# Kernel tuning notes

Hardware: AMD Instinct MI355X
Metric: run time of the kernel (lower is better)

The kernel has to match this reference:

```python
import jax, jax.numpy as jnp
import numpy as np

B = 2
T = 1024
D_MODEL = 1024
EXPAND = 2
D_INNER = D_MODEL * EXPAND  # 2048
D_STATE = 16
D_CONV = 4
DT_RANK = 64  # ceil(1024/16)


def setup_inputs() -> dict:
    key = jax.random.key(0)
    ks = jax.random.split(key, 9)
    s = 0.02
    x = jax.random.normal(ks[0], (B, T, D_MODEL), jnp.float32)
    in_proj_w = jax.random.normal(ks[1], (2 * D_INNER, D_MODEL), jnp.float32) * s
    conv_w = jax.random.normal(ks[2], (D_INNER, 1, D_CONV), jnp.float32) * 0.1
    conv_b = jax.random.normal(ks[3], (D_INNER,), jnp.float32) * 0.01
    x_proj_w = jax.random.normal(ks[4], (DT_RANK + 2 * D_STATE, D_INNER), jnp.float32) * s
    dt_proj_w = jax.random.normal(ks[5], (D_INNER, DT_RANK), jnp.float32) * s
    dt_proj_b = jax.random.uniform(ks[6], (D_INNER,), jnp.float32, -4.0, -2.0)
    A_log = jnp.log(jnp.tile(jnp.arange(1, D_STATE + 1, dtype=jnp.float32), (D_INNER, 1)))
    D_param = jnp.ones((D_INNER,), jnp.float32)
    out_proj_w = jax.random.normal(ks[7], (D_MODEL, D_INNER), jnp.float32) * s
    return {"x": x, "in_proj_w": in_proj_w, "conv_w": conv_w, "conv_b": conv_b,
            "x_proj_w": x_proj_w, "dt_proj_w": dt_proj_w, "dt_proj_b": dt_proj_b,
            "A_log": A_log, "D_param": D_param, "out_proj_w": out_proj_w}


def reference(x, in_proj_w, conv_w, conv_b, x_proj_w, dt_proj_w, dt_proj_b,
              A_log, D_param, out_proj_w):
    Bsz, Tlen, _ = x.shape
    # input projection -> (B,T,2*d_inner); split into x-branch and gate z
    xz = jnp.einsum('btd,ed->bte', x, in_proj_w)
    xs, z = jnp.split(xz, 2, axis=-1)
    # causal depthwise conv1d: torch pads both sides by d_conv-1 then slices [:T],
    # equivalent to left-pad d_conv-1
    xc = jnp.swapaxes(xs, 1, 2)  # (B, d_inner, T)
    xc = jax.lax.conv_general_dilated(xc, conv_w, window_strides=(1,),
                                      padding=[(D_CONV - 1, 0)],
                                      feature_group_count=D_INNER)
    xc = xc + conv_b[None, :, None]
    xs = jax.nn.silu(jnp.swapaxes(xc, 1, 2))  # (B,T,d_inner)
    A = -jnp.exp(A_log)  # (d_inner, d_state)
    x_dbl = jnp.einsum('bti,ei->bte', xs, x_proj_w)
    dt, Bv, Cv = jnp.split(x_dbl, [DT_RANK, DT_RANK + D_STATE], axis=-1)
    dt = jax.nn.softplus(jnp.einsum('btr,ir->bti', dt, dt_proj_w) + dt_proj_b)
    # selective scan: h_t = exp(dt_t*A)*h_{t-1} + (dt_t*x_t)*B_t ; y_t = <h_t, C_t>
    def step(h, inp):
        dt_t, B_t, C_t, x_t = inp  # (B,Di),(B,Ds),(B,Ds),(B,Di)
        dA = jnp.exp(dt_t[:, :, None] * A[None])        # (B,Di,Ds)
        h = dA * h + (dt_t * x_t)[:, :, None] * B_t[:, None, :]
        y_t = jnp.einsum('bds,bs->bd', h, C_t)
        return h, y_t
    tm = lambda a: jnp.swapaxes(a, 0, 1)  # time-major
    h0 = jnp.zeros((Bsz, D_INNER, D_STATE), x.dtype)
    _, ys = jax.lax.scan(step, h0, (tm(dt), tm(Bv), tm(Cv), tm(xs)))
    y = jnp.swapaxes(ys, 0, 1) + xs * D_param  # (B,T,d_inner)
    y = y * jax.nn.silu(z)
    return jnp.einsum('bti,di->btd', y, out_proj_w)
```

## Files before the change

kernel.cpp:

```cpp
#include <hip/hip_runtime.h>
#include <hip/hip_bf16.h>
#include <math.h>

#define B_SZ 2
#define T_LEN 1024
#define DMODEL 1024
#define DINNER 2048
#define DSTATE 16
#define DCONV 4
#define DTRANK 64
#define MTOK (B_SZ * T_LEN)

#define NC 32
#define CLEN (T_LEN / NC)
#define NCH (B_SZ * DINNER)
#define NSTATES (NCH * DSTATE)

typedef __bf16 bf16x4 __attribute__((ext_vector_type(4)));
typedef __bf16 bf16x8 __attribute__((ext_vector_type(8)));
typedef float  f32x4  __attribute__((ext_vector_type(4)));

__device__ __forceinline__ float sigmoid_f(float v) { return 1.f / (1.f + __expf(-v)); }

__global__ __launch_bounds__(256) void convert3(const float* __restrict__ x,
                                                const float* __restrict__ w_in,
                                                const float* __restrict__ w_out,
                                                __bf16* __restrict__ xb,
                                                __bf16* __restrict__ wb_in,
                                                __bf16* __restrict__ wb_out)
{
    const int gi = blockIdx.x * blockDim.x + threadIdx.x;
    const float* src; __bf16* dst; int o;
    if (gi < 262144)            { src = x;     dst = xb;     o = gi; }
    else if (gi < 786432)       { src = w_in;  dst = wb_in;  o = gi - 262144; }
    else                        { src = w_out; dst = wb_out; o = gi - 786432; }
    float4 a = reinterpret_cast<const float4*>(src)[2 * o];
    float4 b = reinterpret_cast<const float4*>(src)[2 * o + 1];
    bf16x8 v = {(__bf16)a.x, (__bf16)a.y, (__bf16)a.z, (__bf16)a.w,
                (__bf16)b.x, (__bf16)b.y, (__bf16)b.z, (__bf16)b.w};
    reinterpret_cast<bf16x8*>(dst)[o] = v;
}

template<int BN, typename CT>
__global__ __launch_bounds__(256) void mfma_gemm_bf16(const __bf16* __restrict__ A, int lda,
                                                      const __bf16* __restrict__ Bm, int ldb,
                                                      CT* __restrict__ C, int ldc, int K)
{
    constexpr int NF = BN / 32;
    constexpr int BCALLS = BN / 32;
    __shared__ __align__(16) __bf16 As[128 * 64];
    __shared__ __align__(16) __bf16 Bs[BN * 64];
    const int tid  = threadIdx.x;
    const int lane = tid & 63;
    const int w    = tid >> 6;
    const int wr   = w >> 1, wc = w & 1;
    const int m0   = blockIdx.y * 128, n0 = blockIdx.x * BN;

    f32x4 acc[4][NF];
    #pragma unroll
    for (int i = 0; i < 4; ++i)
        #pragma unroll
        for (int j = 0; j < NF; ++j) {
            f32x4 z = {0.f, 0.f, 0.f, 0.f};
            acc[i][j] = z;
        }

    const int fr = lane & 15;
    const int kq = (lane >> 4) * 8;

    for (int k0 = 0; k0 < K; k0 += 64) {
        #pragma unroll
        for (int c = 0; c < 4; ++c) {
            const int idx = c * 256 + tid;
            const int row = idx >> 3;
            const int kc  = (idx & 7) * 8;
            __builtin_amdgcn_global_load_lds(
                (const __attribute__((address_space(1))) unsigned int*)(A + (size_t)(m0 + row) * lda + k0 + kc),
                (__attribute__((address_space(3))) unsigned int*)(As + idx * 8),
                16, 0, 0);
        }
        #pragma unroll
        for (int c = 0; c < BCALLS; ++c) {
            const int idx = c * 256 + tid;
            const int row = idx >> 3;
            const int kc  = (idx & 7) * 8;
            __builtin_amdgcn_global_load_lds(
                (const __attribute__((address_space(1))) unsigned int*)(Bm + (size_t)(n0 + row) * ldb + k0 + kc),
                (__attribute__((address_space(3))) unsigned int*)(Bs + idx * 8),
                16, 0, 0);
        }
        __syncthreads();

        bf16x8 af[4][2], bfr[NF][2];
        #pragma unroll
        for (int i = 0; i < 4; ++i) {
            const __bf16* pa = As + (wr * 64 + i * 16 + fr) * 64 + kq;
            af[i][0] = *reinterpret_cast<const bf16x8*>(pa);
            af[i][1] = *reinterpret_cast<const bf16x8*>(pa + 32);
        }
        #pragma unroll
        for (int j = 0; j < NF; ++j) {
            const __bf16* pb = Bs + (wc * (BN / 2) + j * 16 + fr) * 64 + kq;
            bfr[j][0] = *reinterpret_cast<const bf16x8*>(pb);
            bfr[j][1] = *reinterpret_cast<const bf16x8*>(pb + 32);
        }
        #pragma unroll
        for (int i = 0; i < 4; ++i)
            #pragma unroll
            for (int j = 0; j < NF; ++j) {
                acc[i][j] = __builtin_amdgcn_mfma_f32_16x16x32_bf16(af[i][0], bfr[j][0], acc[i][j], 0, 0, 0);
                acc[i][j] = __builtin_amdgcn_mfma_f32_16x16x32_bf16(af[i][1], bfr[j][1], acc[i][j], 0, 0, 0);
            }
        __syncthreads();
    }

    const int crow = (lane >> 4) * 4;
    const int ccol = lane & 15;
    #pragma unroll
    for (int i = 0; i < 4; ++i)
        #pragma unroll
        for (int j = 0; j < NF; ++j) {
            CT* cp = C + (size_t)(m0 + wr * 64 + i * 16 + crow) * ldc
                       + n0 + wc * (BN / 2) + j * 16 + ccol;
            cp[0 * (size_t)ldc] = (CT)acc[i][j][0];
            cp[1 * (size_t)ldc] = (CT)acc[i][j][1];
            cp[2 * (size_t)ldc] = (CT)acc[i][j][2];
            cp[3 * (size_t)ldc] = (CT)acc[i][j][3];
        }
}

__global__ __launch_bounds__(256) void gemm_dtproj(const float* __restrict__ A,
                                                   const float* __restrict__ Bm,
                                                   __bf16* __restrict__ C,
                                                   const float* __restrict__ bias)
{
    __shared__ float As[16][68];
    __shared__ float Bs[16][68];
    const int tx = threadIdx.x & 15;
    const int ty = threadIdx.x >> 4;
    const int m0 = blockIdx.y * 64;
    const int n0 = blockIdx.x * 64;
    const int lr = threadIdx.x >> 2;
    const int lc = (threadIdx.x & 3) * 4;

    float acc[4][4] = {};

    for (int k0 = 0; k0 < DTRANK; k0 += 16) {
        {
            float4 v = *reinterpret_cast<const float4*>(&A[(size_t)(m0 + lr) * 96 + k0 + lc]);
            As[lc + 0][lr] = v.x; As[lc + 1][lr] = v.y;
            As[lc + 2][lr] = v.z; As[lc + 3][lr] = v.w;
        }
        {
            float4 v = *reinterpret_cast<const float4*>(&Bm[(size_t)(n0 + lr) * DTRANK + k0 + lc]);
            Bs[lc + 0][lr] = v.x; Bs[lc + 1][lr] = v.y;
            Bs[lc + 2][lr] = v.z; Bs[lc + 3][lr] = v.w;
        }
        __syncthreads();
        #pragma unroll
        for (int kk = 0; kk < 16; ++kk) {
            float av[4], bv[4];
            #pragma unroll
            for (int i = 0; i < 4; ++i) av[i] = As[kk][ty + 16 * i];
            #pragma unroll
            for (int j = 0; j < 4; ++j) bv[j] = Bs[kk][tx + 16 * j];
            #pragma unroll
            for (int i = 0; i < 4; ++i)
                #pragma unroll
                for (int j = 0; j < 4; ++j)
                    acc[i][j] = fmaf(av[i], bv[j], acc[i][j]);
        }
        __syncthreads();
    }

    #pragma unroll
    for (int i = 0; i < 4; ++i) {
        int m = m0 + ty + 16 * i;
        #pragma unroll
        for (int j = 0; j < 4; ++j) {
            int n = n0 + tx + 16 * j;
            float v = acc[i][j] + bias[n];
            v = (v > 20.f) ? v : log1pf(__expf(v));
            C[(size_t)m * DINNER + n] = (__bf16)v;
        }
    }
}

#define XP_KS 16
#define XP_KC (DINNER / XP_KS)

__global__ __launch_bounds__(256) void gemm_xproj_splitk(const __bf16* __restrict__ xsb,
                                                         const float* __restrict__ W,
                                                         float* __restrict__ pbuf)
{
    __shared__ float As[16][68];
    __shared__ float Bs[16][68];
    const int tx = threadIdx.x & 15;
    const int ty = threadIdx.x >> 4;
    const int n0 = blockIdx.x * 64;
    const int m0 = blockIdx.y * 64;
    const int kz = blockIdx.z;
    const int lr = threadIdx.x >> 2;
    const int lc = (threadIdx.x & 3) * 4;

    float acc[4][4] = {};

    for (int k0 = kz * XP_KC; k0 < (kz + 1) * XP_KC; k0 += 16) {
        {
            bf16x4 v = *reinterpret_cast<const bf16x4*>(&xsb[(size_t)(m0 + lr) * DINNER + k0 + lc]);
            As[lc + 0][lr] = (float)v[0]; As[lc + 1][lr] = (float)v[1];
            As[lc + 2][lr] = (float)v[2]; As[lc + 3][lr] = (float)v[3];
        }
        {
            int n = n0 + lr;
            float4 v = make_float4(0.f, 0.f, 0.f, 0.f);
            if (n < DTRANK + 2 * DSTATE)
                v = *reinterpret_cast<const float4*>(&W[(size_t)n * DINNER + k0 + lc]);
            Bs[lc + 0][lr] = v.x; Bs[lc + 1][lr] = v.y;
            Bs[lc + 2][lr] = v.z; Bs[lc + 3][lr] = v.w;
        }
        __syncthreads();
        #pragma unroll
        for (int kk = 0; kk < 16; ++kk) {
            float av[4], bv[4];
            #pragma unroll
            for (int i = 0; i < 4; ++i) av[i] = As[kk][ty + 16 * i];
            #pragma unroll
            for (int j = 0; j < 4; ++j) bv[j] = Bs[kk][tx + 16 * j];
            #pragma unroll
            for (int i = 0; i < 4; ++i)
                #pragma unroll
                for (int j = 0; j < 4; ++j)
                    acc[i][j] = fmaf(av[i], bv[j], acc[i][j]);
        }
        __syncthreads();
    }

    float* pc = pbuf + (size_t)kz * MTOK * 96;
    #pragma unroll
    for (int i = 0; i < 4; ++i) {
        int m = m0 + ty + 16 * i;
        #pragma unroll
        for (int j = 0; j < 4; ++j) {
            int n = n0 + tx + 16 * j;
            if (n < 96) pc[(size_t)m * 96 + n] = acc[i][j];
        }
    }
}

__global__ __launch_bounds__(256) void reduce_xproj(const float* __restrict__ pbuf,
                                                    float* __restrict__ xdbl)
{
    const int idx = blockIdx.x * blockDim.x + threadIdx.x;
    const float4* p = reinterpret_cast<const float4*>(pbuf) + idx;
    float4 s = p[0];
    #pragma unroll
    for (int z = 1; z < XP_KS; ++z) {
        float4 v = p[(size_t)z * (MTOK * 96 / 4)];
        s.x += v.x; s.y += v.y; s.z += v.z; s.w += v.w;
    }
    reinterpret_cast<float4*>(xdbl)[idx] = s;
}

__global__ __launch_bounds__(256) void conv_silu_kernel(const __bf16* __restrict__ xzb,
                                                        const float* __restrict__ cw,
                                                        const float* __restrict__ cb,
                                                        __bf16* __restrict__ xsb)
{
    int tid = blockIdx.x * blockDim.x + threadIdx.x;
    int d = tid & (DINNER - 1);
    int t = (tid >> 11) & (T_LEN - 1);
    int b = tid >> 21;
    float acc = cb[d];
    const float4 w = *reinterpret_cast<const float4*>(&cw[d * DCONV]);
    float wv[4] = {w.x, w.y, w.z, w.w};
    #pragma unroll
    for (int j = 0; j < DCONV; ++j) {
        int tt = t - (DCONV - 1) + j;
        if (tt >= 0)
            acc = fmaf((float)xzb[((size_t)(b * T_LEN + tt)) * (2 * DINNER) + d], wv[j], acc);
    }
    xsb[tid] = (__bf16)(acc * sigmoid_f(acc));
}

__global__ __launch_bounds__(256) void scan_pass1(const __bf16* __restrict__ dtb,
                                                  const __bf16* __restrict__ xsb,
                                                  const float* __restrict__ xdbl,
                                                  const float* __restrict__ A_log,
                                                  float* __restrict__ Pb,
                                                  float* __restrict__ Bb)
{
    __shared__ float sB[CLEN][16];
    const int tid = threadIdx.x;
    const int g   = blockIdx.x * 256 + tid;
    const int c   = blockIdx.y;
    const int b   = g >> 11;
    const int d   = g & (DINNER - 1);
    const int m0  = b * T_LEN + c * CLEN;

    if (tid < CLEN * 4) {
        int t = tid >> 2, s4 = (tid & 3) * 4;
        *reinterpret_cast<float4*>(&sB[t][s4]) =
            *reinterpret_cast<const float4*>(&xdbl[(size_t)(m0 + t) * 96 + DTRANK + s4]);
    }
    __syncthreads();

    float a[DSTATE], h[DSTATE];
    #pragma unroll
    for (int s4 = 0; s4 < DSTATE; s4 += 4) {
        float4 v = *reinterpret_cast<const float4*>(&A_log[d * DSTATE + s4]);
        a[s4 + 0] = -__expf(v.x); a[s4 + 1] = -__expf(v.y);
        a[s4 + 2] = -__expf(v.z); a[s4 + 3] = -__expf(v.w);
        h[s4 + 0] = 0.f; h[s4 + 1] = 0.f; h[s4 + 2] = 0.f; h[s4 + 3] = 0.f;
    }

    float sumdt = 0.f;
    float dtc = (float)dtb[(size_t)m0 * DINNER + d];
    float xc  = (float)xsb[(size_t)m0 * DINNER + d];
    for (int t = 0; t < CLEN; ++t) {
        float dtn = 0.f, xn = 0.f;
        if (t + 1 < CLEN) {
            dtn = (float)dtb[(size_t)(m0 + t + 1) * DINNER + d];
            xn  = (float)xsb[(size_t)(m0 + t + 1) * DINNER + d];
        }
        sumdt += dtc;
        const float u = dtc * xc;
        #pragma unroll
        for (int s = 0; s < DSTATE; ++s) {
            const float dA = __expf(dtc * a[s]);
            h[s] = fmaf(dA, h[s], u * sB[t][s]);
        }
        dtc = dtn; xc = xn;
    }

    float* pp = Pb + ((size_t)c * NCH + g) * DSTATE;
    float* bp = Bb + ((size_t)c * NCH + g) * DSTATE;
    #pragma unroll
    for (int s4 = 0; s4 < DSTATE; s4 += 4) {
        float4 pv = {__expf(a[s4] * sumdt), __expf(a[s4 + 1] * sumdt),
                     __expf(a[s4 + 2] * sumdt), __expf(a[s4 + 3] * sumdt)};
        *reinterpret_cast<float4*>(pp + s4) = pv;
        float4 hv = {h[s4], h[s4 + 1], h[s4 + 2], h[s4 + 3]};
        *reinterpret_cast<float4*>(bp + s4) = hv;
    }
}

__global__ __launch_bounds__(256) void scan_pass2(const float* __restrict__ Pb,
                                                  float* __restrict__ Bb)
{
    const int idx = blockIdx.x * blockDim.x + threadIdx.x;
    float h = 0.f;
    #pragma unroll
    for (int c = 0; c < NC; ++c) {
        const size_t o = (size_t)c * NSTATES + idx;
        const float P  = Pb[o];
        const float Bv = Bb[o];
        Bb[o] = h;
        h = fmaf(P, h, Bv);
    }
}

__global__ __launch_bounds__(256) void scan_pass3(const __bf16* __restrict__ dtb,
                                                  const __bf16* __restrict__ xsb,
                                                  const float* __restrict__ xdbl,
                                                  const float* __restrict__ Hs,
                                                  const float* __restrict__ A_log,
                                                  const float* __restrict__ Dp,
                                                  const __bf16* __restrict__ xzb,
                                                  __bf16* __restrict__ yMb)
{
    __shared__ float sBC[CLEN][32];
    const int tid = threadIdx.x;
    const int g   = blockIdx.x * 256 + tid;
    const int c   = blockIdx.y;
    const int b   = g >> 11;
    const int d   = g & (DINNER - 1);
    const int m0  = b * T_LEN + c * CLEN;

    {
        int t = tid >> 3, col = (tid & 7) * 4;
        if (t < CLEN)
            *reinterpret_cast<float4*>(&sBC[t][col]) =
                *reinterpret_cast<const float4*>(&xdbl[(size_t)(m0 + t) * 96 + DTRANK + col]);
    }
    __syncthreads();

    float a[DSTATE], h[DSTATE];
    #pragma unroll
    for (int s4 = 0; s4 < DSTATE; s4 += 4) {
        float4 v = *reinterpret_cast<const float4*>(&A_log[d * DSTATE + s4]);
        a[s4 + 0] = -__expf(v.x); a[s4 + 1] = -__expf(v.y);
        a[s4 + 2] = -__expf(v.z); a[s4 + 3] = -__expf(v.w);
        float4 hv = *reinterpret_cast<const float4*>(
            Hs + ((size_t)c * NCH + g) * DSTATE + s4);
        h[s4 + 0] = hv.x; h[s4 + 1] = hv.y; h[s4 + 2] = hv.z; h[s4 + 3] = hv.w;
    }
    const float Dv = Dp[d];

    float dtc = (float)dtb[(size_t)m0 * DINNER + d];
    float xc  = (float)xsb[(size_t)m0 * DINNER + d];
    float zc  = (float)xzb[(size_t)m0 * (2 * DINNER) + DINNER + d];
    for (int t = 0; t < CLEN; ++t) {
        float dtn = 0.f, xn = 0.f, zn = 0.f;
        if (t + 1 < CLEN) {
            dtn = (float)dtb[(size_t)(m0 + t + 1) * DINNER + d];
            xn  = (float)xsb[(size_t)(m0 + t + 1) * DINNER + d];
            zn  = (float)xzb[(size_t)(m0 + t + 1) * (2 * DINNER) + DINNER + d];
        }
        const float u = dtc * xc;
        float y0 = 0.f, y1 = 0.f, y2 = 0.f, y3 = 0.f;
        #pragma unroll
        for (int s = 0; s < DSTATE; s += 4) {
            float dA0 = __expf(dtc * a[s + 0]);
            float dA1 = __expf(dtc * a[s + 1]);
            float dA2 = __expf(dtc * a[s + 2]);
            float dA3 = __expf(dtc * a[s + 3]);
            h[s + 0] = fmaf(dA0, h[s + 0], u * sBC[t][s + 0]);
            h[s + 1] = fmaf(dA1, h[s + 1], u * sBC[t][s + 1]);
            h[s + 2] = fmaf(dA2, h[s + 2], u * sBC[t][s + 2]);
            h[s + 3] = fmaf(dA3, h[s + 3], u * sBC[t][s + 3]);
            y0 = fmaf(h[s + 0], sBC[t][16 + s + 0], y0);
            y1 = fmaf(h[s + 1], sBC[t][16 + s + 1], y1);
            y2 = fmaf(h[s + 2], sBC[t][16 + s + 2], y2);
            y3 = fmaf(h[s + 3], sBC[t][16 + s + 3], y3);
        }
        float y = (y0 + y1) + (y2 + y3) + xc * Dv;
        const float gate = zc * sigmoid_f(zc);
        yMb[(size_t)(m0 + t) * DINNER + d] = (__bf16)(y * gate);
        dtc = dtn; xc = xn; zc = zn;
    }
}

extern "C" void kernel_launch(void* const* d_in, const int* in_sizes, int n_in,
                              void* d_out, int out_size, void* d_ws, size_t ws_size,
                              hipStream_t stream) {
    const float* x         = (const float*)d_in[0];
    const float* in_proj_w = (const float*)d_in[1];
    const float* conv_w    = (const float*)d_in[2];
    const float* conv_b    = (const float*)d_in[3];
    const float* x_proj_w  = (const float*)d_in[4];
    const float* dt_proj_w = (const float*)d_in[5];
    const float* dt_proj_b = (const float*)d_in[6];
    const float* A_log     = (const float*)d_in[7];
    const float* D_param   = (const float*)d_in[8];
    const float* out_proj_w= (const float*)d_in[9];
    float* out = (float*)d_out;

    float* ws = (float*)d_ws;
    const size_t M1 = (size_t)1024 * 1024;
    __bf16* xzb    = (__bf16*)ws;
    __bf16* xb     = (__bf16*)(ws + 4 * M1);
    __bf16* wb_in  = (__bf16*)(ws + 5 * M1);
    __bf16* wb_out = (__bf16*)(ws + 7 * M1);
    __bf16* xsb    = (__bf16*)(ws + 8 * M1);
    __bf16* dtb    = (__bf16*)(ws + 10 * M1);
    float*  xdbl   = ws + 12 * M1;
    float*  pbuf   = ws + 13 * M1;
    float*  Pb     = ws + 16 * M1;
    float*  Bb     = ws + 18 * M1;
    __bf16* yMb    = (__bf16*)(ws + 20 * M1);

    dim3 blk(256);

    convert3<<<dim3(4096), blk, 0, stream>>>(x, in_proj_w, out_proj_w, xb, wb_in, wb_out);

    mfma_gemm_bf16<128, __bf16><<<dim3((2 * DINNER) / 128, MTOK / 128), blk, 0, stream>>>(
        xb, DMODEL, wb_in, DMODEL, xzb, 2 * DINNER, DMODEL);

    conv_silu_kernel<<<dim3(B_SZ * T_LEN * DINNER / 256), blk, 0, stream>>>(xzb, conv_w, conv_b, xsb);

    gemm_xproj_splitk<<<dim3(2, MTOK / 64, XP_KS), blk, 0, stream>>>(xsb, x_proj_w, pbuf);

    reduce_xproj<<<dim3(MTOK * 96 / 4 / 256), blk, 0, stream>>>(pbuf, xdbl);

    gemm_dtproj<<<dim3(DINNER / 64, MTOK / 64), blk, 0, stream>>>(xdbl, dt_proj_w, dtb, dt_proj_b);

    scan_pass1<<<dim3(NCH / 256, NC), blk, 0, stream>>>(dtb, xsb, xdbl, A_log, Pb, Bb);
    scan_pass2<<<dim3(NSTATES / 256), blk, 0, stream>>>(Pb, Bb);
    scan_pass3<<<dim3(NCH / 256, NC), blk, 0, stream>>>(dtb, xsb, xdbl, Bb, A_log, D_param, xzb, yMb);

    mfma_gemm_bf16<64, float><<<dim3(DMODEL / 64, MTOK / 128), blk, 0, stream>>>(
        yMb, DINNER, wb_out, DINNER, out, DMODEL, DINNER);
}
```

Before: 194.2 us.

## Fuse conv+SiLU into x_proj and scan kernels, replace split-K reduce with atomics

Removes the standalone conv_silu kernel and its xsb buffer. The depthwise causal conv and SiLU are now recomputed on the fly from xzb inside the x_proj GEMM load path and inside both scan passes, using a sliding window of three previous values. The split-K partial buffer and its reduce kernel are replaced by atomic adds into xdbl, which is zeroed by extra blocks of the convert kernel. This saves two launches and a large intermediate write and read, at the cost of redundant conv arithmetic, four-times-wider loads in the GEMM tile fill, and nondeterministic float atomics.

```diff
diff --git a/kernel.cpp b/kernel.cpp
--- a/kernel.cpp
+++ b/kernel.cpp
@@ -27,13 +27,21 @@
                                                 const float* __restrict__ w_out,
                                                 __bf16* __restrict__ xb,
                                                 __bf16* __restrict__ wb_in,
-                                                __bf16* __restrict__ wb_out)
+                                                __bf16* __restrict__ wb_out,
+                                                float* __restrict__ xdbl)
 {
     const int gi = blockIdx.x * blockDim.x + threadIdx.x;
+    if (gi >= 1048576) {
+        const int o = gi - 1048576;
+        float4 z = make_float4(0.f, 0.f, 0.f, 0.f);
+        reinterpret_cast<float4*>(xdbl)[2 * o]     = z;
+        reinterpret_cast<float4*>(xdbl)[2 * o + 1] = z;
+        return;
+    }
     const float* src; __bf16* dst; int o;
-    if (gi < 262144)            { src = x;     dst = xb;     o = gi; }
-    else if (gi < 786432)       { src = w_in;  dst = wb_in;  o = gi - 262144; }
-    else                        { src = w_out; dst = wb_out; o = gi - 786432; }
+    if (gi < 262144)      { src = x;     dst = xb;     o = gi; }
+    else if (gi < 786432) { src = w_in;  dst = wb_in;  o = gi - 262144; }
+    else                  { src = w_out; dst = wb_out; o = gi - 786432; }
     float4 a = reinterpret_cast<const float4*>(src)[2 * o];
     float4 b = reinterpret_cast<const float4*>(src)[2 * o + 1];
     bf16x8 v = {(__bf16)a.x, (__bf16)a.y, (__bf16)a.z, (__bf16)a.w,
@@ -129,69 +137,14 @@
         }
 }
 
-__global__ __launch_bounds__(256) void gemm_dtproj(const float* __restrict__ A,
-                                                   const float* __restrict__ Bm,
-                                                   __bf16* __restrict__ C,
-                                                   const float* __restrict__ bias)
-{
-    __shared__ float As[16][68];
-    __shared__ float Bs[16][68];
-    const int tx = threadIdx.x & 15;
-    const int ty = threadIdx.x >> 4;
-    const int m0 = blockIdx.y * 64;
-    const int n0 = blockIdx.x * 64;
-    const int lr = threadIdx.x >> 2;
-    const int lc = (threadIdx.x & 3) * 4;
-
-    float acc[4][4] = {};
-
-    for (int k0 = 0; k0 < DTRANK; k0 += 16) {
-        {
-            float4 v = *reinterpret_cast<const float4*>(&A[(size_t)(m0 + lr) * 96 + k0 + lc]);
-            As[lc + 0][lr] = v.x; As[lc + 1][lr] = v.y;
-            As[lc + 2][lr] = v.z; As[lc + 3][lr] = v.w;
-        }
-        {
-            float4 v = *reinterpret_cast<const float4*>(&Bm[(size_t)(n0 + lr) * DTRANK + k0 + lc]);
-            Bs[lc + 0][lr] = v.x; Bs[lc + 1][lr] = v.y;
-            Bs[lc + 2][lr] = v.z; Bs[lc + 3][lr] = v.w;
-        }
-        __syncthreads();
-        #pragma unroll
-        for (int kk = 0; kk < 16; ++kk) {
-            float av[4], bv[4];
-            #pragma unroll
-            for (int i = 0; i < 4; ++i) av[i] = As[kk][ty + 16 * i];
-            #pragma unroll
-            for (int j = 0; j < 4; ++j) bv[j] = Bs[kk][tx + 16 * j];
-            #pragma unroll
-            for (int i = 0; i < 4; ++i)
-                #pragma unroll
-                for (int j = 0; j < 4; ++j)
-                    acc[i][j] = fmaf(av[i], bv[j], acc[i][j]);
-        }
-        __syncthreads();
-    }
-
-    #pragma unroll
-    for (int i = 0; i < 4; ++i) {
-        int m = m0 + ty + 16 * i;
-        #pragma unroll
-        for (int j = 0; j < 4; ++j) {
-            int n = n0 + tx + 16 * j;
-            float v = acc[i][j] + bias[n];
-            v = (v > 20.f) ? v : log1pf(__expf(v));
-            C[(size_t)m * DINNER + n] = (__bf16)v;
-        }
-    }
-}
-
 #define XP_KS 16
 #define XP_KC (DINNER / XP_KS)
 
-__global__ __launch_bounds__(256) void gemm_xproj_splitk(const __bf16* __restrict__ xsb,
+__global__ __launch_bounds__(256) void gemm_xproj_splitk(const __bf16* __restrict__ xzb,
+                                                         const float* __restrict__ cw,
+                                                         const float* __restrict__ cb,
                                                          const float* __restrict__ W,
-                                                         float* __restrict__ pbuf)
+                                                         float* __restrict__ xdbl)
 {
     __shared__ float As[16][68];
     __shared__ float Bs[16][68];
@@ -203,13 +156,38 @@
     const int lr = threadIdx.x >> 2;
     const int lc = (threadIdx.x & 3) * 4;
 
+    const int m  = m0 + lr;
+    const int tb = m & (T_LEN - 1);
+
     float acc[4][4] = {};
 
     for (int k0 = kz * XP_KC; k0 < (kz + 1) * XP_KC; k0 += 16) {
         {
-            bf16x4 v = *reinterpret_cast<const bf16x4*>(&xsb[(size_t)(m0 + lr) * DINNER + k0 + lc]);
-            As[lc + 0][lr] = (float)v[0]; As[lc + 1][lr] = (float)v[1];
-            As[lc + 2][lr] = (float)v[2]; As[lc + 3][lr] = (float)v[3];
+            const int ch0 = k0 + lc;
+            float xv[4][4];
+            #pragma unroll
+            for (int j = 0; j < 4; ++j) {
+                if (tb - 3 + j >= 0) {
+                    bf16x4 v = *reinterpret_cast<const bf16x4*>(
+                        &xzb[(size_t)(m - 3 + j) * (2 * DINNER) + ch0]);
+                    xv[j][0] = (float)v[0]; xv[j][1] = (float)v[1];
+                    xv[j][2] = (float)v[2]; xv[j][3] = (float)v[3];
+                } else {
+                    xv[j][0] = xv[j][1] = xv[j][2] = xv[j][3] = 0.f;
+                }
+            }
+            float4 cbv = *reinterpret_cast<const float4*>(&cb[ch0]);
+            float cbw[4] = {cbv.x, cbv.y, cbv.z, cbv.w};
+            #pragma unroll
+            for (int c = 0; c < 4; ++c) {
+                float4 wv = *reinterpret_cast<const float4*>(&cw[(ch0 + c) * DCONV]);
+                float a = cbw[c];
+                a = fmaf(xv[0][c], wv.x, a);
+                a = fmaf(xv[1][c], wv.y, a);
+                a = fmaf(xv[2][c], wv.z, a);
+                a = fmaf(xv[3][c], wv.w, a);
+                As[lc + c][lr] = a * sigmoid_f(a);
+            }
         }
         {
             int n = n0 + lr;
@@ -236,55 +214,78 @@
         __syncthreads();
     }
 
-    float* pc = pbuf + (size_t)kz * MTOK * 96;
+    #pragma unroll
+    for (int i = 0; i < 4; ++i) {
+        int mm = m0 + ty + 16 * i;
+        #pragma unroll
+        for (int j = 0; j < 4; ++j) {
+            int n = n0 + tx + 16 * j;
+            if (n < 96) unsafeAtomicAdd(&xdbl[(size_t)mm * 96 + n], acc[i][j]);
+        }
+    }
+}
+
+__global__ __launch_bounds__(256) void gemm_dtproj(const float* __restrict__ A,
+                                                   const float* __restrict__ Bm,
+                                                   __bf16* __restrict__ C,
+                                                   const float* __restrict__ bias)
+{
+    __shared__ float As[16][68];
+    __shared__ float Bs[16][68];
+    const int tx = threadIdx.x & 15;
+    const int ty = threadIdx.x >> 4;
+    const int m0 = blockIdx.y * 64;
+    const int n0 = blockIdx.x * 64;
+    const int lr = threadIdx.x >> 2;
+    const int lc = (threadIdx.x & 3) * 4;
+
+    float acc[4][4] = {};
+
+    for (int k0 = 0; k0 < DTRANK; k0 += 16) {
+        {
+            float4 v = *reinterpret_cast<const float4*>(&A[(size_t)(m0 + lr) * 96 + k0 + lc]);
+            As[lc + 0][lr] = v.x; As[lc + 1][lr] = v.y;
+            As[lc + 2][lr] = v.z; As[lc + 3][lr] = v.w;
+        }
+        {
+            float4 v = *reinterpret_cast<const float4*>(&Bm[(size_t)(n0 + lr) * DTRANK + k0 + lc]);
+            Bs[lc + 0][lr] = v.x; Bs[lc + 1][lr] = v.y;
+            Bs[lc + 2][lr] = v.z; Bs[lc + 3][lr] = v.w;
+        }
+        __syncthreads();
+        #pragma unroll
+        for (int kk = 0; kk < 16; ++kk) {
+            float av[4], bv[4];
+            #pragma unroll
+            for (int i = 0; i < 4; ++i) av[i] = As[kk][ty + 16 * i];
+            #pragma unroll
+            for (int j = 0; j < 4; ++j) bv[j] = Bs[kk][tx + 16 * j];
+            #pragma unroll
+            for (int i = 0; i < 4; ++i)
+                #pragma unroll
+                for (int j = 0; j < 4; ++j)
+                    acc[i][j] = fmaf(av[i], bv[j], acc[i][j]);
+        }
+        __syncthreads();
+    }
+
     #pragma unroll
     for (int i = 0; i < 4; ++i) {
         int m = m0 + ty + 16 * i;
         #pragma unroll
         for (int j = 0; j < 4; ++j) {
             int n = n0 + tx + 16 * j;
-            if (n < 96) pc[(size_t)m * 96 + n] = acc[i][j];
-        }
-    }
-}
-
-__global__ __launch_bounds__(256) void reduce_xproj(const float* __restrict__ pbuf,
-                                                    float* __restrict__ xdbl)
-{
-    const int idx = blockIdx.x * blockDim.x + threadIdx.x;
-    const float4* p = reinterpret_cast<const float4*>(pbuf) + idx;
-    float4 s = p[0];
-    #pragma unroll
-    for (int z = 1; z < XP_KS; ++z) {
-        float4 v = p[(size_t)z * (MTOK * 96 / 4)];
-        s.x += v.x; s.y += v.y; s.z += v.z; s.w += v.w;
-    }
-    reinterpret_cast<float4*>(xdbl)[idx] = s;
-}
-
-__global__ __launch_bounds__(256) void conv_silu_kernel(const __bf16* __restrict__ xzb,
-                                                        const float* __restrict__ cw,
-                                                        const float* __restrict__ cb,
-                                                        __bf16* __restrict__ xsb)
-{
-    int tid = blockIdx.x * blockDim.x + threadIdx.x;
-    int d = tid & (DINNER - 1);
-    int t = (tid >> 11) & (T_LEN - 1);
-    int b = tid >> 21;
-    float acc = cb[d];
-    const float4 w = *reinterpret_cast<const float4*>(&cw[d * DCONV]);
-    float wv[4] = {w.x, w.y, w.z, w.w};
-    #pragma unroll
-    for (int j = 0; j < DCONV; ++j) {
-        int tt = t - (DCONV - 1) + j;
-        if (tt >= 0)
-            acc = fmaf((float)xzb[((size_t)(b * T_LEN + tt)) * (2 * DINNER) + d], wv[j], acc);
-    }
-    xsb[tid] = (__bf16)(acc * sigmoid_f(acc));
+            float v = acc[i][j] + bias[n];
+            v = (v > 20.f) ? v : log1pf(__expf(v));
+            C[(size_t)m * DINNER + n] = (__bf16)v;
+        }
+    }
 }
 
 __global__ __launch_bounds__(256) void scan_pass1(const __bf16* __restrict__ dtb,
-                                                  const __bf16* __restrict__ xsb,
+                                                  const __bf16* __restrict__ xzb,
+                                                  const float* __restrict__ cw,
+                                                  const float* __restrict__ cb,
                                                   const float* __restrict__ xdbl,
                                                   const float* __restrict__ A_log,
                                                   float* __restrict__ Pb,
@@ -314,15 +315,28 @@
         h[s4 + 0] = 0.f; h[s4 + 1] = 0.f; h[s4 + 2] = 0.f; h[s4 + 3] = 0.f;
     }
 
+    const float4 wv = *reinterpret_cast<const float4*>(&cw[d * DCONV]);
+    const float cbv = cb[d];
+    float xw0, xw1, xw2;
+    if (c > 0) {
+        xw0 = (float)xzb[(size_t)(m0 - 3) * (2 * DINNER) + d];
+        xw1 = (float)xzb[(size_t)(m0 - 2) * (2 * DINNER) + d];
+        xw2 = (float)xzb[(size_t)(m0 - 1) * (2 * DINNER) + d];
+    } else { xw0 = xw1 = xw2 = 0.f; }
+
     float sumdt = 0.f;
     float dtc = (float)dtb[(size_t)m0 * DINNER + d];
-    float xc  = (float)xsb[(size_t)m0 * DINNER + d];
+    float xzc = (float)xzb[(size_t)m0 * (2 * DINNER) + d];
     for (int t = 0; t < CLEN; ++t) {
-        float dtn = 0.f, xn = 0.f;
+        float dtn = 0.f, xzn = 0.f;
         if (t + 1 < CLEN) {
             dtn = (float)dtb[(size_t)(m0 + t + 1) * DINNER + d];
-            xn  = (float)xsb[(size_t)(m0 + t + 1) * DINNER + d];
-        }
+            xzn = (float)xzb[(size_t)(m0 + t + 1) * (2 * DINNER) + d];
+        }
+        float xc = cbv;
+        xc = fmaf(xw0, wv.x, xc); xc = fmaf(xw1, wv.y, xc);
+        xc = fmaf(xw2, wv.z, xc); xc = fmaf(xzc, wv.w, xc);
+        xc = xc * sigmoid_f(xc);
         sumdt += dtc;
         const float u = dtc * xc;
         #pragma unroll
@@ -330,7 +344,8 @@
             const float dA = __expf(dtc * a[s]);
             h[s] = fmaf(dA, h[s], u * sB[t][s]);
         }
-        dtc = dtn; xc = xn;
+        xw0 = xw1; xw1 = xw2; xw2 = xzc;
+        dtc = dtn; xzc = xzn;
     }
 
     float* pp = Pb + ((size_t)c * NCH + g) * DSTATE;
@@ -361,12 +376,13 @@
 }
 
 __global__ __launch_bounds__(256) void scan_pass3(const __bf16* __restrict__ dtb,
-                                                  const __bf16* __restrict__ xsb,
+                                                  const __bf16* __restrict__ xzb,
+                                                  const float* __restrict__ cw,
+                                                  const float* __restrict__ cb,
                                                   const float* __restrict__ xdbl,
                                                   const float* __restrict__ Hs,
                                                   const float* __restrict__ A_log,
                                                   const float* __restrict__ Dp,
-                                                  const __bf16* __restrict__ xzb,
                                                   __bf16* __restrict__ yMb)
 {
     __shared__ float sBC[CLEN][32];
@@ -397,16 +413,29 @@
     }
     const float Dv = Dp[d];
 
+    const float4 wv = *reinterpret_cast<const float4*>(&cw[d * DCONV]);
+    const float cbv = cb[d];
+    float xw0, xw1, xw2;
+    if (c > 0) {
+        xw0 = (float)xzb[(size_t)(m0 - 3) * (2 * DINNER) + d];
+        xw1 = (float)xzb[(size_t)(m0 - 2) * (2 * DINNER) + d];
+        xw2 = (float)xzb[(size_t)(m0 - 1) * (2 * DINNER) + d];
+    } else { xw0 = xw1 = xw2 = 0.f; }
+
     float dtc = (float)dtb[(size_t)m0 * DINNER + d];
-    float xc  = (float)xsb[(size_t)m0 * DINNER + d];
+    float xzc = (float)xzb[(size_t)m0 * (2 * DINNER) + d];
     float zc  = (float)xzb[(size_t)m0 * (2 * DINNER) + DINNER + d];
     for (int t = 0; t < CLEN; ++t) {
-        float dtn = 0.f, xn = 0.f, zn = 0.f;
+        float dtn = 0.f, xzn = 0.f, zn = 0.f;
         if (t + 1 < CLEN) {
             dtn = (float)dtb[(size_t)(m0 + t + 1) * DINNER + d];
-            xn  = (float)xsb[(size_t)(m0 + t + 1) * DINNER + d];
+            xzn = (float)xzb[(size_t)(m0 + t + 1) * (2 * DINNER) + d];
             zn  = (float)xzb[(size_t)(m0 + t + 1) * (2 * DINNER) + DINNER + d];
         }
+        float xc = cbv;
+        xc = fmaf(xw0, wv.x, xc); xc = fmaf(xw1, wv.y, xc);
+        xc = fmaf(xw2, wv.z, xc); xc = fmaf(xzc, wv.w, xc);
+        xc = xc * sigmoid_f(xc);
         const float u = dtc * xc;
         float y0 = 0.f, y1 = 0.f, y2 = 0.f, y3 = 0.f;
         #pragma unroll
@@ -427,7 +456,8 @@
         float y = (y0 + y1) + (y2 + y3) + xc * Dv;
         const float gate = zc * sigmoid_f(zc);
         yMb[(size_t)(m0 + t) * DINNER + d] = (__bf16)(y * gate);
-        dtc = dtn; xc = xn; zc = zn;
+        xw0 = xw1; xw1 = xw2; xw2 = xzc;
+        dtc = dtn; xzc = xzn; zc = zn;
     }
 }
 
@@ -452,32 +482,27 @@
     __bf16* xb     = (__bf16*)(ws + 4 * M1);
     __bf16* wb_in  = (__bf16*)(ws + 5 * M1);
     __bf16* wb_out = (__bf16*)(ws + 7 * M1);
-    __bf16* xsb    = (__bf16*)(ws + 8 * M1);
-    __bf16* dtb    = (__bf16*)(ws + 10 * M1);
-    float*  xdbl   = ws + 12 * M1;
-    float*  pbuf   = ws + 13 * M1;
-    float*  Pb     = ws + 16 * M1;
-    float*  Bb     = ws + 18 * M1;
-    __bf16* yMb    = (__bf16*)(ws + 20 * M1);
+    __bf16* dtb    = (__bf16*)(ws + 8 * M1);
+    float*  xdbl   = ws + 10 * M1;
+    float*  Pb     = ws + 11 * M1;
+    float*  Bb     = ws + 13 * M1;
+    __bf16* yMb    = (__bf16*)(ws + 15 * M1);
 
     dim3 blk(256);
 
-    convert3<<<dim3(4096), blk, 0, stream>>>(x, in_proj_w, out_proj_w, xb, wb_in, wb_out);
+    convert3<<<dim3(4192), blk, 0, stream>>>(x, in_proj_w, out_proj_w, xb, wb_in, wb_out, xdbl);
 
     mfma_gemm_bf16<128, __bf16><<<dim3((2 * DINNER) / 128, MTOK / 128), blk, 0, stream>>>(
         xb, DMODEL, wb_in, DMODEL, xzb, 2 * DINNER, DMODEL);
 
-    conv_silu_kernel<<<dim3(B_SZ * T_LEN * DINNER / 256), blk, 0, stream>>>(xzb, conv_w, conv_b, xsb);
-
-    gemm_xproj_splitk<<<dim3(2, MTOK / 64, XP_KS), blk, 0, stream>>>(xsb, x_proj_w, pbuf);
-
-    reduce_xproj<<<dim3(MTOK * 96 / 4 / 256), blk, 0, stream>>>(pbuf, xdbl);
+    gemm_xproj_splitk<<<dim3(2, MTOK / 64, XP_KS), blk, 0, stream>>>(
+        xzb, conv_w, conv_b, x_proj_w, xdbl);
 
     gemm_dtproj<<<dim3(DINNER / 64, MTOK / 64), blk, 0, stream>>>(xdbl, dt_proj_w, dtb, dt_proj_b);
 
-    scan_pass1<<<dim3(NCH / 256, NC), blk, 0, stream>>>(dtb, xsb, xdbl, A_log, Pb, Bb);
+    scan_pass1<<<dim3(NCH / 256, NC), blk, 0, stream>>>(dtb, xzb, conv_w, conv_b, xdbl, A_log, Pb, Bb);
     scan_pass2<<<dim3(NSTATES / 256), blk, 0, stream>>>(Pb, Bb);
-    scan_pass3<<<dim3(NCH / 256, NC), blk, 0, stream>>>(dtb, xsb, xdbl, Bb, A_log, D_param, xzb, yMb);
+    scan_pass3<<<dim3(NCH / 256, NC), blk, 0, stream>>>(dtb, xzb, conv_w, conv_b, xdbl, Bb, A_log, D_param, yMb);
 
     mfma_gemm_bf16<64, float><<<dim3(DMODEL / 64, MTOK / 128), blk, 0, stream>>>(
         yMb, DINNER, wb_out, DINNER, out, DMODEL, DINNER);
```

Measured after the change: 194.5 us. No clear change (+0.2%).

## Replace FP32 split-K x_proj GEMM and reduction with bf16 MFMA atomic split-K

Applied to the files above, without the earlier changes.

The x_proj projection moves from a scalar FP32 split-K GEMM with a separate reduce kernel to a bf16 MFMA kernel. It loads tiles straight into LDS and accumulates split-K partials into xdbl with float atomics. The x_proj weight conversion to bf16 and the zeroing of xdbl are folded into the existing conversion kernel. This removes one launch and the partial-sum buffer traffic, at the cost of atomic contention, non-deterministic summation order and lower weight precision.

```diff
diff --git a/kernel.cpp b/kernel.cpp
--- a/kernel.cpp
+++ b/kernel.cpp
@@ -16,24 +16,38 @@
 #define NCH (B_SZ * DINNER)
 #define NSTATES (NCH * DSTATE)
 
+#define XPK 8
+#define XPKC (DINNER / XPK)
+
 typedef __bf16 bf16x4 __attribute__((ext_vector_type(4)));
 typedef __bf16 bf16x8 __attribute__((ext_vector_type(8)));
 typedef float  f32x4  __attribute__((ext_vector_type(4)));
 
 __device__ __forceinline__ float sigmoid_f(float v) { return 1.f / (1.f + __expf(-v)); }
 
-__global__ __launch_bounds__(256) void convert3(const float* __restrict__ x,
+__global__ __launch_bounds__(256) void convert4(const float* __restrict__ x,
                                                 const float* __restrict__ w_in,
                                                 const float* __restrict__ w_out,
+                                                const float* __restrict__ w_xp,
                                                 __bf16* __restrict__ xb,
                                                 __bf16* __restrict__ wb_in,
-                                                __bf16* __restrict__ wb_out)
+                                                __bf16* __restrict__ wb_out,
+                                                __bf16* __restrict__ wxp,
+                                                float* __restrict__ xdbl)
 {
     const int gi = blockIdx.x * blockDim.x + threadIdx.x;
+    if (gi >= 1073152) {
+        const int o = gi - 1073152;
+        float4 z = make_float4(0.f, 0.f, 0.f, 0.f);
+        reinterpret_cast<float4*>(xdbl)[2 * o]     = z;
+        reinterpret_cast<float4*>(xdbl)[2 * o + 1] = z;
+        return;
+    }
     const float* src; __bf16* dst; int o;
-    if (gi < 262144)            { src = x;     dst = xb;     o = gi; }
-    else if (gi < 786432)       { src = w_in;  dst = wb_in;  o = gi - 262144; }
-    else                        { src = w_out; dst = wb_out; o = gi - 786432; }
+    if (gi < 262144)       { src = x;     dst = xb;     o = gi; }
+    else if (gi < 786432)  { src = w_in;  dst = wb_in;  o = gi - 262144; }
+    else if (gi < 1048576) { src = w_out; dst = wb_out; o = gi - 786432; }
+    else                   { src = w_xp;  dst = wxp;    o = gi - 1048576; }
     float4 a = reinterpret_cast<const float4*>(src)[2 * o];
     float4 b = reinterpret_cast<const float4*>(src)[2 * o + 1];
     bf16x8 v = {(__bf16)a.x, (__bf16)a.y, (__bf16)a.z, (__bf16)a.w,
@@ -127,6 +141,101 @@
             cp[2 * (size_t)ldc] = (CT)acc[i][j][2];
             cp[3 * (size_t)ldc] = (CT)acc[i][j][3];
         }
+}
+
+__global__ __launch_bounds__(256) void mfma_xproj(const __bf16* __restrict__ A,
+                                                  const __bf16* __restrict__ Bm,
+                                                  float* __restrict__ xdbl)
+{
+    __shared__ __align__(16) __bf16 As[128 * 64];
+    __shared__ __align__(16) __bf16 Bs[32 * 64];
+    const int tid  = threadIdx.x;
+    const int lane = tid & 63;
+    const int w    = tid >> 6;
+    const int wr   = w >> 1, wc = w & 1;
+    const int m0   = blockIdx.y * 128, n0 = blockIdx.x * 32;
+    const int kbeg = blockIdx.z * XPKC;
+
+    f32x4 acc[4];
+    #pragma unroll
+    for (int i = 0; i < 4; ++i) { f32x4 z = {0.f, 0.f, 0.f, 0.f}; acc[i] = z; }
+
+    const int fr = lane & 15;
+    const int kq = (lane >> 4) * 8;
+
+    for (int k0 = kbeg; k0 < kbeg + XPKC; k0 += 64) {
+        #pragma unroll
+        for (int c = 0; c < 4; ++c) {
+            const int idx = c * 256 + tid;
+            const int row = idx >> 3;
+            const int kc  = (idx & 7) * 8;
+            __builtin_amdgcn_global_load_lds(
+                (const __attribute__((address_space(1))) unsigned int*)(A + (size_t)(m0 + row) * DINNER + k0 + kc),
+                (__attribute__((address_space(3))) unsigned int*)(As + idx * 8),
+                16, 0, 0);
+        }
+        {
+            const int row = tid >> 3;
+            const int kc  = (tid & 7) * 8;
+            __builtin_amdgcn_global_load_lds(
+                (const __attribute__((address_space(1))) unsigned int*)(Bm + (size_t)(n0 + row) * DINNER + k0 + kc),
+                (__attribute__((address_space(3))) unsigned int*)(Bs + tid * 8),
+                16, 0, 0);
+        }
+        __syncthreads();
+
+        bf16x8 af[4][2], bfr[2];
+        #pragma unroll
+        for (int i = 0; i < 4; ++i) {
+            const __bf16* pa = As + (wr * 64 + i * 16 + fr) * 64 + kq;
+            af[i][0] = *reinterpret_cast<const bf16x8*>(pa);
+            af[i][1] = *reinterpret_cast<const bf16x8*>(pa + 32);
+        }
+        {
+            const __bf16* pb = Bs + (wc * 16 + fr) * 64 + kq;
+            bfr[0] = *reinterpret_cast<const bf16x8*>(pb);
+            bfr[1] = *reinterpret_cast<const bf16x8*>(pb + 32);
+        }
+        #pragma unroll
+        for (int i = 0; i < 4; ++i) {
+            acc[i] = __builtin_amdgcn_mfma_f32_16x16x32_bf16(af[i][0], bfr[0], acc[i], 0, 0, 0);
+            acc[i] = __builtin_amdgcn_mfma_f32_16x16x32_bf16(af[i][1], bfr[1], acc[i], 0, 0, 0);
+        }
+        __syncthreads();
+    }
+
+    const int crow = (lane >> 4) * 4;
+    const int ccol = lane & 15;
+    const int n = n0 + wc * 16 + ccol;
+    #pragma unroll
+    for (int i = 0; i < 4; ++i) {
+        const int m = m0 + wr * 64 + i * 16 + crow;
+        unsafeAtomicAdd(&xdbl[(size_t)(m + 0) * 96 + n], acc[i][0]);
+        unsafeAtomicAdd(&xdbl[(size_t)(m + 1) * 96 + n], acc[i][1]);
+        unsafeAtomicAdd(&xdbl[(size_t)(m + 2) * 96 + n], acc[i][2]);
+        unsafeAtomicAdd(&xdbl[(size_t)(m + 3) * 96 + n], acc[i][3]);
+    }
+}
+
+__global__ __launch_bounds__(256) void conv_silu_kernel(const __bf16* __restrict__ xzb,
+                                                        const float* __restrict__ cw,
+                                                        const float* __restrict__ cb,
+                                                        __bf16* __restrict__ xsb)
+{
+    int tid = blockIdx.x * blockDim.x + threadIdx.x;
+    int d = tid & (DINNER - 1);
+    int t = (tid >> 11) & (T_LEN - 1);
+    int b = tid >> 21;
+    float acc = cb[d];
+    const float4 w = *reinterpret_cast<const float4*>(&cw[d * DCONV]);
+    float wv[4] = {w.x, w.y, w.z, w.w};
+    #pragma unroll
+    for (int j = 0; j < DCONV; ++j) {
+        int tt = t - (DCONV - 1) + j;
+        if (tt >= 0)
+            acc = fmaf((float)xzb[((size_t)(b * T_LEN + tt)) * (2 * DINNER) + d], wv[j], acc);
+    }
+    xsb[tid] = (__bf16)(acc * sigmoid_f(acc));
 }
 
 __global__ __launch_bounds__(256) void gemm_dtproj(const float* __restrict__ A,
@@ -184,103 +293,6 @@
             C[(size_t)m * DINNER + n] = (__bf16)v;
         }
     }
-}
-
-#define XP_KS 16
-#define XP_KC (DINNER / XP_KS)
-
-__global__ __launch_bounds__(256) void gemm_xproj_splitk(const __bf16* __restrict__ xsb,
-                                                         const float* __restrict__ W,
-                                                         float* __restrict__ pbuf)
-{
-    __shared__ float As[16][68];
-    __shared__ float Bs[16][68];
-    const int tx = threadIdx.x & 15;
-    const int ty = threadIdx.x >> 4;
-    const int n0 = blockIdx.x * 64;
-    const int m0 = blockIdx.y * 64;
-    const int kz = blockIdx.z;
-    const int lr = threadIdx.x >> 2;
-    const int lc = (threadIdx.x & 3) * 4;
-
-    float acc[4][4] = {};
-
-    for (int k0 = kz * XP_KC; k0 < (kz + 1) * XP_KC; k0 += 16) {
-        {
-            bf16x4 v = *reinterpret_cast<const bf16x4*>(&xsb[(size_t)(m0 + lr) * DINNER + k0 + lc]);
-            As[lc + 0][lr] = (float)v[0]; As[lc + 1][lr] = (float)v[1];
-            As[lc + 2][lr] = (float)v[2]; As[lc + 3][lr] = (float)v[3];
-        }
-        {
-            int n = n0 + lr;
-            float4 v = make_float4(0.f, 0.f, 0.f, 0.f);
-            if (n < DTRANK + 2 * DSTATE)
-                v = *reinterpret_cast<const float4*>(&W[(size_t)n * DINNER + k0 + lc]);
-            Bs[lc + 0][lr] = v.x; Bs[lc + 1][lr] = v.y;
-            Bs[lc + 2][lr] = v.z; Bs[lc + 3][lr] = v.w;
-        }
-        __syncthreads();
-        #pragma unroll
-        for (int kk = 0; kk < 16; ++kk) {
-            float av[4], bv[4];
-            #pragma unroll
-            for (int i = 0; i < 4; ++i) av[i] = As[kk][ty + 16 * i];
-            #pragma unroll
-            for (int j = 0; j < 4; ++j) bv[j] = Bs[kk][tx + 16 * j];
-            #pragma unroll
-            for (int i = 0; i < 4; ++i)
-                #pragma unroll
-                for (int j = 0; j < 4; ++j)
-                    acc[i][j] = fmaf(av[i], bv[j], acc[i][j]);
-        }
-        __syncthreads();
-    }
-
-    float* pc = pbuf + (size_t)kz * MTOK * 96;
-    #pragma unroll
-    for (int i = 0; i < 4; ++i) {
-        int m = m0 + ty + 16 * i;
-        #pragma unroll
-        for (int j = 0; j < 4; ++j) {
-            int n = n0 + tx + 16 * j;
-            if (n < 96) pc[(size_t)m * 96 + n] = acc[i][j];
-        }
-    }
-}
-
-__global__ __launch_bounds__(256) void reduce_xproj(const float* __restrict__ pbuf,
-                                                    float* __restrict__ xdbl)
-{
-    const int idx = blockIdx.x * blockDim.x + threadIdx.x;
-    const float4* p = reinterpret_cast<const float4*>(pbuf) + idx;
-    float4 s = p[0];
-    #pragma unroll
-    for (int z = 1; z < XP_KS; ++z) {
-        float4 v = p[(size_t)z * (MTOK * 96 / 4)];
-        s.x += v.x; s.y += v.y; s.z += v.z; s.w += v.w;
-    }
-    reinterpret_cast<float4*>(xdbl)[idx] = s;
-}
-
-__global__ __launch_bounds__(256) void conv_silu_kernel(const __bf16* __restrict__ xzb,
-                                                        const float* __restrict__ cw,
-                                                        const float* __restrict__ cb,
-                                                        __bf16* __restrict__ xsb)
-{
-    int tid = blockIdx.x * blockDim.x + threadIdx.x;
-    int d = tid & (DINNER - 1);
-    int t = (tid >> 11) & (T_LEN - 1);
-    int b = tid >> 21;
-    float acc = cb[d];
-    const float4 w = *reinterpret_cast<const float4*>(&cw[d * DCONV]);
-    float wv[4] = {w.x, w.y, w.z, w.w};
-    #pragma unroll
-    for (int j = 0; j < DCONV; ++j) {
-        int tt = t - (DCONV - 1) + j;
-        if (tt >= 0)
-            acc = fmaf((float)xzb[((size_t)(b * T_LEN + tt)) * (2 * DINNER) + d], wv[j], acc);
-    }
-    xsb[tid] = (__bf16)(acc * sigmoid_f(acc));
 }
 
 __global__ __launch_bounds__(256) void scan_pass1(const __bf16* __restrict__ dtb,
@@ -452,26 +464,25 @@
     __bf16* xb     = (__bf16*)(ws + 4 * M1);
     __bf16* wb_in  = (__bf16*)(ws + 5 * M1);
     __bf16* wb_out = (__bf16*)(ws + 7 * M1);
-    __bf16* xsb    = (__bf16*)(ws + 8 * M1);
-    __bf16* dtb    = (__bf16*)(ws + 10 * M1);
-    float*  xdbl   = ws + 12 * M1;
-    float*  pbuf   = ws + 13 * M1;
-    float*  Pb     = ws + 16 * M1;
-    float*  Bb     = ws + 18 * M1;
-    __bf16* yMb    = (__bf16*)(ws + 20 * M1);
+    __bf16* wxp    = (__bf16*)(ws + 8 * M1);
+    __bf16* xsb    = (__bf16*)(ws + 9 * M1);
+    __bf16* dtb    = (__bf16*)(ws + 11 * M1);
+    float*  xdbl   = ws + 13 * M1;
+    float*  Pb     = ws + 14 * M1;
+    float*  Bb     = ws + 16 * M1;
+    __bf16* yMb    = (__bf16*)(ws + 18 * M1);
 
     dim3 blk(256);
 
-    convert3<<<dim3(4096), blk, 0, stream>>>(x, in_proj_w, out_proj_w, xb, wb_in, wb_out);
+    convert4<<<dim3(4288), blk, 0, stream>>>(x, in_proj_w, out_proj_w, x_proj_w,
+                                             xb, wb_in, wb_out, wxp, xdbl);
 
     mfma_gemm_bf16<128, __bf16><<<dim3((2 * DINNER) / 128, MTOK / 128), blk, 0, stream>>>(
         xb, DMODEL, wb_in, DMODEL, xzb, 2 * DINNER, DMODEL);
 
     conv_silu_kernel<<<dim3(B_SZ * T_LEN * DINNER / 256), blk, 0, stream>>>(xzb, conv_w, conv_b, xsb);
 
-    gemm_xproj_splitk<<<dim3(2, MTOK / 64, XP_KS), blk, 0, stream>>>(xsb, x_proj_w, pbuf);
-
-    reduce_xproj<<<dim3(MTOK * 96 / 4 / 256), blk, 0, stream>>>(pbuf, xdbl);
+    mfma_xproj<<<dim3(3, MTOK / 128, XPK), blk, 0, stream>>>(xsb, wxp, xdbl);
 
     gemm_dtproj<<<dim3(DINNER / 64, MTOK / 64), blk, 0, stream>>>(xdbl, dt_proj_w, dtb, dt_proj_b);
 
```

After: 177.9 us (median of 2 runs). 1.09x faster.
